# Kernel optimization log

Hardware: AMD Instinct MI355X
Metric: run time of the kernel (lower is better)

The kernel has to match this reference:

```python
import jax, jax.numpy as jnp
import numpy as np

D_MODEL = 1024
EXPAND = 2
D_INNER = D_MODEL * EXPAND  # 2048
D_STATE = 16
D_CONV = 4
B, T = 4, 2048


def setup_inputs() -> dict:
    key = jax.random.key(0)
    ks = jax.random.split(key, 8)
    s = 0.02  # small init std for numeric stability
    return {
        "x": jax.random.normal(ks[0], (B, T, D_MODEL), jnp.float32),
        "in_proj_w": jax.random.normal(ks[1], (2 * D_INNER, D_MODEL), jnp.float32) * s,
        "conv_w": jax.random.normal(ks[2], (D_INNER, 1, D_CONV), jnp.float32) * s,
        "conv_b": jnp.zeros((D_INNER,), jnp.float32),
        "x_proj_w": jax.random.normal(ks[3], (2 * D_STATE, D_INNER), jnp.float32) * s,
        "dt_proj_w": jax.random.normal(ks[4], (D_INNER, D_STATE), jnp.float32) * s,
        "dt_proj_b": jnp.zeros((D_INNER,), jnp.float32),
        "D_param": jnp.ones((D_INNER,), jnp.float32),
        "out_proj_w": jax.random.normal(ks[5], (D_MODEL, D_INNER), jnp.float32) * s,
    }


def reference(x, in_proj_w, conv_w, conv_b, x_proj_w, dt_proj_w, dt_proj_b, D_param, out_proj_w):
    Bsz, Tlen, _ = x.shape
    # in_proj (no bias), torch Linear: x @ W.T
    xz = jnp.einsum('btd,ed->bte', x, in_proj_w)            # [B,T,2*D_INNER]
    x_inner, z = jnp.split(xz, 2, axis=-1)                   # each [B,T,D_INNER]
    # depthwise causal conv1d: left-pad d_conv-1, take first T outputs
    xc = jnp.transpose(x_inner, (0, 2, 1))                   # [B,D_INNER,T]
    xc = jax.lax.conv_general_dilated(
        xc, conv_w, window_strides=(1,), padding=[(D_CONV - 1, 0)],
        feature_group_count=D_INNER)
    xc = xc + conv_b[None, :, None]
    x_conv = jax.nn.silu(jnp.transpose(xc, (0, 2, 1)))       # [B,T,D_INNER]
    # x_proj -> (B_ssm, C_ssm); C_ssm is unused by the simplified scan (faithful)
    x_ssm = jnp.einsum('btd,ed->bte', x_conv, x_proj_w)      # [B,T,2*D_STATE]
    B_ssm, C_ssm = jnp.split(x_ssm, 2, axis=-1)
    dt = jax.nn.softplus(jnp.einsum('btn,dn->btd', B_ssm, dt_proj_w) + dt_proj_b)  # [B,T,D_INNER]
    # simplified selective scan: EMA with scalar-per-timestep gate
    alpha = jax.nn.sigmoid(jnp.mean(dt, axis=-1, keepdims=True))  # [B,T,1]

    def step(h, inp):
        a, xt = inp
        h = a * h + (1.0 - a) * xt
        return h, h

    aT = jnp.transpose(alpha, (1, 0, 2))   # [T,B,1]
    xT = jnp.transpose(x_conv, (1, 0, 2))  # [T,B,D_INNER]
    h0 = jnp.zeros((Bsz, D_INNER), x.dtype)
    _, ys = jax.lax.scan(step, h0, (aT, xT))
    y = jnp.transpose(ys, (1, 0, 2))        # [B,T,D_INNER]
    y = y * D_param + x_conv                # skip with learned D
    y = y * jax.nn.silu(z)                  # gate
    out = jnp.einsum('btd,ed->bte', y, out_proj_w)  # [B,T,D_MODEL]
    return out
```

## Files before the change

kernel.cpp:

```cpp
#include <hip/hip_runtime.h>
#include <stdint.h>

#define TLEN   2048
#define DMODEL 1024
#define DINNER 2048
#define MROWS  8192
#define NCH    64
#define CHUNK  32

typedef unsigned short u16;
typedef __bf16 bf16x8 __attribute__((ext_vector_type(8)));
typedef float  f32x4  __attribute__((ext_vector_type(4)));

__device__ __forceinline__ float bf2f(u16 u) {
  union { unsigned int i; float f; } v; v.i = ((unsigned int)u) << 16; return v.f;
}
__device__ __forceinline__ u16 f2bf(float f) {
  union { float f; unsigned int u; } v; v.f = f;
  unsigned int u = v.u;
  return (u16)((u + 0x7fffu + ((u >> 16) & 1u)) >> 16);
}
__device__ __forceinline__ float silu_f(float x) { return x / (1.f + __expf(-x)); }

__device__ __forceinline__ void async16(const u16* g, u16* l) {
  __builtin_amdgcn_global_load_lds(
      (const __attribute__((address_space(1))) void*)(g),
      (__attribute__((address_space(3))) void*)(l),
      16, 0, 0);
}

#define BAR      asm volatile("s_barrier" ::: "memory")
#define WAITV(n) asm volatile("s_waitcnt vmcnt(" #n ")" ::: "memory")
#define PRIO1    __builtin_amdgcn_s_setprio(1)
#define PRIO0    __builtin_amdgcn_s_setprio(0)

__global__ __launch_bounds__(256) void k_convert(const float* __restrict__ x,
    const float* __restrict__ w1, const float* __restrict__ w3,
    const float* __restrict__ xpw,
    u16* __restrict__ xb, u16* __restrict__ w1b, u16* __restrict__ w3b,
    u16* __restrict__ xpwb) {
  int i = blockIdx.x * 256 + threadIdx.x;
  const int nx  = MROWS * DMODEL / 4;
  const int nw1 = 2 * DINNER * DMODEL / 4;
  const int nw3 = DMODEL * DINNER / 4;
  const float* src; u16* dst; int j;
  if (i < nx)                  { src = x;   dst = xb;   j = i; }
  else if (i < nx + nw1)       { src = w1;  dst = w1b;  j = i - nx; }
  else if (i < nx + nw1 + nw3) { src = w3;  dst = w3b;  j = i - nx - nw1; }
  else                         { src = xpw; dst = xpwb; j = i - nx - nw1 - nw3; }
  float4 v = ((const float4*)src)[j];
  ushort4 o;
  o.x = f2bf(v.x); o.y = f2bf(v.y); o.z = f2bf(v.z); o.w = f2bf(v.w);
  ((ushort4*)dst)[j] = o;
}

__device__ __forceinline__ u16* regp(u16* lds, int s, int mat, int h) {
  return lds + (((s * 2 + mat) * 2 + h) * 8192);
}

__device__ __forceinline__ void read_a(bf16x8 (&dst)[4][2], const u16* reg,
                                       int qa, int fr, int c0, int c1) {
  #pragma unroll
  for (int m = 0; m < 4; m++) {
    const u16* p = reg + (qa * 64 + m * 16 + fr) * 64;
    dst[m][0] = *(const bf16x8*)(p + c0);
    dst[m][1] = *(const bf16x8*)(p + c1);
  }
}
__device__ __forceinline__ void read_b(bf16x8 (&dst)[2][2], const u16* reg,
                                       int rb, int c0, int c1) {
  #pragma unroll
  for (int n = 0; n < 2; n++) {
    const u16* p = reg + (rb + n * 16) * 64;
    dst[n][0] = *(const bf16x8*)(p + c0);
    dst[n][1] = *(const bf16x8*)(p + c1);
  }
}
__device__ __forceinline__ void mfma_quad(f32x4 (&acc)[8][4],
    const bf16x8 (&af)[4][2], const bf16x8 (&bf)[2][2], int qa, int qb) {
  #pragma unroll
  for (int m = 0; m < 4; m++)
    #pragma unroll
    for (int n = 0; n < 2; n++)
      #pragma unroll
      for (int ks = 0; ks < 2; ks++)
        acc[qa * 4 + m][qb * 2 + n] = __builtin_amdgcn_mfma_f32_16x16x32_bf16(
            af[m][ks], bf[n][ks], acc[qa * 4 + m][qb * 2 + n], 0, 0, 0);
}

template<int N, int K, bool OUT_BF16>
__global__ __launch_bounds__(512) void k_gemm8p(const u16* __restrict__ A,
    const u16* __restrict__ Bm, void* __restrict__ C) {
  static_assert(K % 128 == 0, "K must be multiple of 128");
  extern __shared__ u16 lds[];
  const int tid  = threadIdx.x;
  const int lane = tid & 63;
  const int wave = tid >> 6;
  const int wm   = wave >> 2;
  const int wn   = wave & 3;
  const int fr   = lane & 15;
  const int q    = lane >> 4;

  int wg = blockIdx.x, nwg = gridDim.x, swz = wg;
  if ((nwg & 7) == 0) swz = (wg & 7) * (nwg >> 3) + (wg >> 3);
  const int NT_N = N / 256;
  const size_t blockM = (size_t)(swz / NT_N) * 256;
  const size_t blockN = (size_t)(swz % NT_N) * 256;

  const int rsub   = tid >> 3;
  const int srcCol = 8 * ((tid & 7) ^ (rsub & 7));
  const u16* gA = A  + (blockM + rsub) * (size_t)K + srcCol;
  const u16* gB = Bm + (blockN + rsub) * (size_t)K + srcCol;

#define STAGE(sl, mat, h, kt) do {                                           \
    const u16* _g = ((mat) ? gB : gA) + (size_t)(h) * (128 * (size_t)K)      \
                    + (size_t)(kt) * 64;                                     \
    u16* _l = regp(lds, (sl), (mat), (h)) + tid * 8;                         \
    async16(_g, _l);                                                         \
    async16(_g + (size_t)64 * K, _l + 4096);                                 \
  } while (0)

  const int c0 = (((q * 16)      ^ ((fr & 7) << 4)) >> 1);
  const int c1 = (((64 + q * 16) ^ ((fr & 7) << 4)) >> 1);
  const int rb = (wn & 1) * 64 + fr;

  f32x4 acc[8][4] = {};
  bf16x8 a0[4][2], a1[4][2], bl[2][2], bh[2][2];

  const int NT = K / 64;
  const int NITER = K / 128;

  STAGE(0, 0, 0, 0); STAGE(0, 0, 1, 0); STAGE(0, 1, 0, 0); STAGE(0, 1, 1, 0);
  STAGE(1, 1, 0, 1); STAGE(1, 1, 1, 1); STAGE(1, 0, 0, 1);
  WAITV(6);
  BAR;

  for (int it = 0; it < NITER; ++it) {
    const int t2 = 2 * it + 2, t3 = 2 * it + 3;
    const bool pf = (t2 < NT);
    read_a(a0, regp(lds, 0, 0, wm), 0, fr, c0, c1);
    read_b(bl, regp(lds, 0, 1, wn >> 1), rb, c0, c1);
    STAGE(1, 0, 1, 2 * it + 1);
    BAR;
    PRIO1; mfma_quad(acc, a0, bl, 0, 0); PRIO0;
    BAR;
    read_b(bh, regp(lds, 0, 1, wn >> 1), rb + 32, c0, c1);
    if (pf) STAGE(0, 1, 0, t2);
    BAR;
    PRIO1; mfma_quad(acc, a0, bh, 0, 1); PRIO0;
    BAR;
    read_a(a1, regp(lds, 0, 0, wm), 1, fr, c0, c1);
    if (pf) STAGE(0, 1, 1, t2);
    BAR;
    PRIO1; mfma_quad(acc, a1, bl, 1, 0); PRIO0;
    BAR;
    if (pf) STAGE(0, 0, 0, t2);
    BAR;
    PRIO1; mfma_quad(acc, a1, bh, 1, 1); PRIO0;
    if (pf) { WAITV(6); } else { WAITV(0); }
    BAR;
    read_a(a0, regp(lds, 1, 0, wm), 0, fr, c0, c1);
    read_b(bl, regp(lds, 1, 1, wn >> 1), rb, c0, c1);
    if (pf) STAGE(0, 0, 1, t2);
    BAR;
    PRIO1; mfma_quad(acc, a0, bl, 0, 0); PRIO0;
    BAR;
    read_b(bh, regp(lds, 1, 1, wn >> 1), rb + 32, c0, c1);
    if (pf) STAGE(1, 1, 0, t3);
    BAR;
    PRIO1; mfma_quad(acc, a0, bh, 0, 1); PRIO0;
    BAR;
    read_a(a1, regp(lds, 1, 0, wm), 1, fr, c0, c1);
    if (pf) STAGE(1, 1, 1, t3);
    BAR;
    PRIO1; mfma_quad(acc, a1, bl, 1, 0); PRIO0;
    BAR;
    if (pf) STAGE(1, 0, 0, t3);
    BAR;
    PRIO1; mfma_quad(acc, a1, bh, 1, 1); PRIO0;
    if (pf) { WAITV(6); BAR; } else { BAR; }
  }
#undef STAGE

  {
    const size_t r0  = blockM + (size_t)wm * 128;
    const size_t cc0 = blockN + (size_t)wn * 64;
    #pragma unroll
    for (int m = 0; m < 8; m++)
      #pragma unroll
      for (int n = 0; n < 4; n++)
        #pragma unroll
        for (int r = 0; r < 4; r++) {
          size_t row = r0 + m * 16 + q * 4 + r;
          size_t col = cc0 + n * 16 + fr;
          float v = acc[m][n][r];
          if (OUT_BF16) ((u16*)C)[row * N + col] = f2bf(v);
          else          ((float*)C)[row * N + col] = v;
        }
  }
}

template<int N, int K, bool OUT_BF16>
__global__ __launch_bounds__(512) void k_gemm_sk(const u16* __restrict__ A,
    const u16* __restrict__ B, void* __restrict__ C) {
  __shared__ u16 smem[2][2][2][4096];
  const int tid   = threadIdx.x;
  const int lane  = tid & 63;
  const int wave8 = tid >> 6;
  const int kw    = wave8 >> 2;
  const int wave  = wave8 & 3;
  const int wm    = (wave >> 1) * 64;
  const int wn    = (wave & 1) * 64;
  const int fr    = lane & 15;
  const int q     = lane >> 4;
  const size_t blockM = (size_t)blockIdx.y * 128;
  const size_t blockN = (size_t)blockIdx.x * 128;

  const int srow = lane >> 2;
  const int scol = (lane & 3) * 8;
  const size_t kbase = (size_t)kw * (K / 2);
  const u16* gA = A + (blockM + (size_t)wave * 32 + srow) * (size_t)K + kbase + scol;
  const u16* gB = B + (blockN + (size_t)wave * 32 + srow) * (size_t)K + kbase + scol;
  u16* lA0 = smem[kw][0][0] + wave * 1024;
  u16* lA1 = smem[kw][0][1] + wave * 1024;
  u16* lB0 = smem[kw][1][0] + wave * 1024;
  u16* lB1 = smem[kw][1][1] + wave * 1024;

  f32x4 acc[4][4] = {};

  for (int kt = 0; kt < K / 2; kt += 64) {
    async16(gA + kt,                        lA0);
    async16(gA + 16 * (size_t)K + kt,       lA0 + 512);
    async16(gA + kt + 32,                   lA1);
    async16(gA + 16 * (size_t)K + kt + 32,  lA1 + 512);
    async16(gB + kt,                        lB0);
    async16(gB + 16 * (size_t)K + kt,       lB0 + 512);
    async16(gB + kt + 32,                   lB1);
    async16(gB + 16 * (size_t)K + kt + 32,  lB1 + 512);
    __syncthreads();

    #pragma unroll
    for (int h = 0; h < 2; h++) {
      bf16x8 af[4], bfr[4];
      #pragma unroll
      for (int tm = 0; tm < 4; tm++)
        af[tm] = *(const bf16x8*)(smem[kw][0][h] + (wm + tm * 16 + fr) * 32 + q * 8);
      #pragma unroll
      for (int tn = 0; tn < 4; tn++)
        bfr[tn] = *(const bf16x8*)(smem[kw][1][h] + (wn + tn * 16 + fr) * 32 + q * 8);
      #pragma unroll
      for (int tm = 0; tm < 4; tm++)
        #pragma unroll
        for (int tn = 0; tn < 4; tn++)
          acc[tm][tn] = __builtin_amdgcn_mfma_f32_16x16x32_bf16(
              af[tm], bfr[tn], acc[tm][tn], 0, 0, 0);
    }
    __syncthreads();
  }

  float* red = (float*)smem;
  if (kw == 1) {
    const int t2 = tid - 256;
    #pragma unroll
    for (int tm = 0; tm < 4; tm++)
      #pragma unroll
      for (int tn = 0; tn < 4; tn++)
        #pragma unroll
        for (int r = 0; r < 4; r++)
          red[((t2 * 4 + tm) * 4 + tn) * 4 + r] = acc[tm][tn][r];
  }
  __syncthreads();
  if (kw == 0) {
    #pragma unroll
    for (int tm = 0; tm < 4; tm++)
      #pragma unroll
      for (int tn = 0; tn < 4; tn++)
        #pragma unroll
        for (int r = 0; r < 4; r++) {
          float v = acc[tm][tn][r] + red[((tid * 4 + tm) * 4 + tn) * 4 + r];
          size_t row = blockM + wm + tm * 16 + q * 4 + r;
          size_t col = blockN + wn + tn * 16 + fr;
          if (OUT_BF16) ((u16*)C)[row * N + col] = f2bf(v);
          else          ((float*)C)[row * N + col] = v;
        }
  }
}

__global__ __launch_bounds__(256) void k_conv(const u16* __restrict__ xz,
    const float* __restrict__ cw, const float* __restrict__ cb,
    u16* __restrict__ xc) {
  const int tb = blockIdx.x & 255;
  const int b  = blockIdx.x >> 8;
  const int d0 = threadIdx.x * 8;

  float wgt[8][4], bias[8];
  #pragma unroll
  for (int j = 0; j < 8; j++) {
    float4 wv = ((const float4*)cw)[d0 + j];
    wgt[j][0] = wv.x; wgt[j][1] = wv.y; wgt[j][2] = wv.z; wgt[j][3] = wv.w;
    bias[j] = cb[d0 + j];
  }

  const int t0 = tb * 8;
  const u16* base = xz + ((size_t)(b * TLEN + t0)) * 4096 + d0;
  float win[3][8];
  #pragma unroll
  for (int k = 0; k < 3; k++) {
    const int t = t0 - 3 + k;
    if (t >= 0) {
      bf16x8 v = *(const bf16x8*)(base + (ptrdiff_t)(k - 3) * 4096);
      #pragma unroll
      for (int j = 0; j < 8; j++) win[k][j] = bf2f(((u16*)&v)[j]);
    } else {
      #pragma unroll
      for (int j = 0; j < 8; j++) win[k][j] = 0.f;
    }
  }

  u16* outp = xc + ((size_t)(b * TLEN + t0)) * DINNER + d0;
  #pragma unroll
  for (int i = 0; i < 8; i++) {
    bf16x8 v = *(const bf16x8*)(base + (ptrdiff_t)i * 4096);
    float cur[8];
    #pragma unroll
    for (int j = 0; j < 8; j++) cur[j] = bf2f(((u16*)&v)[j]);
    union { u16 a[8]; int4 v4; } o;
    #pragma unroll
    for (int j = 0; j < 8; j++) {
      float acc = bias[j] + wgt[j][0] * win[0][j] + wgt[j][1] * win[1][j]
                + wgt[j][2] * win[2][j] + wgt[j][3] * cur[j];
      o.a[j] = f2bf(silu_f(acc));
    }
    *(int4*)(outp + (size_t)i * DINNER) = o.v4;
    #pragma unroll
    for (int j = 0; j < 8; j++) { win[0][j] = win[1][j]; win[1][j] = win[2][j]; win[2][j] = cur[j]; }
  }
}

__global__ __launch_bounds__(256) void k_bssm(const u16* __restrict__ xc,
    const u16* __restrict__ xpwb, float* __restrict__ bssm) {
  const int tid  = threadIdx.x;
  const int lane = tid & 63;
  const int wave = tid >> 6;
  const int fr   = lane & 15;
  const int q    = lane >> 4;
  const size_t row0 = (size_t)blockIdx.x * 32;
  const int k0 = wave * 512;

  f32x4 acc[2] = {};
  #pragma unroll
  for (int kk = 0; kk < 512; kk += 32) {
    const int kb = k0 + kk + q * 8;
    bf16x8 bfrag = *(const bf16x8*)(xpwb + (size_t)fr * DINNER + kb);
    #pragma unroll
    for (int tm = 0; tm < 2; tm++) {
      bf16x8 afrag = *(const bf16x8*)(xc + (row0 + tm * 16 + fr) * (size_t)DINNER + kb);
      acc[tm] = __builtin_amdgcn_mfma_f32_16x16x32_bf16(afrag, bfrag, acc[tm], 0, 0, 0);
    }
  }

  __shared__ float red[4][32][16];
  #pragma unroll
  for (int tm = 0; tm < 2; tm++)
    #pragma unroll
    for (int r = 0; r < 4; r++)
      red[wave][tm * 16 + q * 4 + r][fr] = acc[tm][r];
  __syncthreads();
  #pragma unroll
  for (int i = tid; i < 512; i += 256) {
    int r = i >> 4, n = i & 15;
    bssm[(row0 + r) * 16 + n] =
        red[0][r][n] + red[1][r][n] + red[2][r][n] + red[3][r][n];
  }
}

__global__ __launch_bounds__(256) void k_alpha(const float* __restrict__ bssm,
    const float* __restrict__ dtw, const float* __restrict__ dtb,
    float* __restrict__ alpha) {
  const int tid = threadIdx.x;
  const size_t row0 = (size_t)blockIdx.x * 16;
  __shared__ float4 sB[16][4];
  { int r = tid >> 4, n = tid & 15;
    ((float*)&sB[r][0])[n] = bssm[(row0 + r) * 16 + n]; }
  __syncthreads();

  float rowsum[16];
  #pragma unroll
  for (int r = 0; r < 16; r++) rowsum[r] = 0.f;

  #pragma unroll 1
  for (int m = 0; m < 4; m++) {
    const int d0 = m * 512 + tid * 2;
    float4 w[2][4]; float bias[2];
    #pragma unroll
    for (int j = 0; j < 2; j++) {
      const float4* wp = (const float4*)(dtw + (size_t)(d0 + j) * 16);
      w[j][0] = wp[0]; w[j][1] = wp[1]; w[j][2] = wp[2]; w[j][3] = wp[3];
      bias[j] = dtb[d0 + j];
    }
    #pragma unroll
    for (int r = 0; r < 16; r++) {
      float4 b0 = sB[r][0], b1 = sB[r][1], b2 = sB[r][2], b3 = sB[r][3];
      float s = 0.f;
      #pragma unroll
      for (int j = 0; j < 2; j++) {
        float dot = bias[j]
          + b0.x * w[j][0].x + b0.y * w[j][0].y + b0.z * w[j][0].z + b0.w * w[j][0].w
          + b1.x * w[j][1].x + b1.y * w[j][1].y + b1.z * w[j][1].z + b1.w * w[j][1].w
          + b2.x * w[j][2].x + b2.y * w[j][2].y + b2.z * w[j][2].z + b2.w * w[j][2].w
          + b3.x * w[j][3].x + b3.y * w[j][3].y + b3.z * w[j][3].z + b3.w * w[j][3].w;
        s += (dot > 15.f) ? dot : __logf(1.f + __expf(dot));
      }
      rowsum[r] += s;
    }
  }
  #pragma unroll
  for (int r = 0; r < 16; r++)
    #pragma unroll
    for (int off = 32; off > 0; off >>= 1) rowsum[r] += __shfl_xor(rowsum[r], off);
  __shared__ float red[4][16];
  if ((tid & 63) == 0) {
    #pragma unroll
    for (int r = 0; r < 16; r++) red[tid >> 6][r] = rowsum[r];
  }
  __syncthreads();
  if (tid < 16) {
    float mean = (red[0][tid] + red[1][tid] + red[2][tid] + red[3][tid]) * (1.f / DINNER);
    alpha[row0 + tid] = 1.f / (1.f + __expf(-mean));
  }
}

__global__ __launch_bounds__(256) void k_scan1(const u16* __restrict__ xc,
    const float* __restrict__ alpha, float* __restrict__ carry) {
  const int c = blockIdx.x & 63;
  const int b = blockIdx.x >> 6;
  const int d0 = threadIdx.x * 8;
  __shared__ float sa[CHUNK];
  if (threadIdx.x < CHUNK) sa[threadIdx.x] = alpha[b * TLEN + c * CHUNK + threadIdx.x];
  __syncthreads();
  const u16* xp = xc + ((size_t)(b * TLEN + c * CHUNK)) * DINNER + d0;
  float h[8];
  #pragma unroll
  for (int j = 0; j < 8; j++) h[j] = 0.f;
  #pragma unroll 4
  for (int i = 0; i < CHUNK; i++) {
    bf16x8 v = *(const bf16x8*)(xp + (size_t)i * DINNER);
    float a = sa[i];
    #pragma unroll
    for (int j = 0; j < 8; j++) h[j] = a * h[j] + (1.f - a) * bf2f(((u16*)&v)[j]);
  }
  float* cp = carry + ((size_t)(b * NCH + c)) * DINNER + d0;
  #pragma unroll
  for (int j = 0; j < 8; j++) cp[j] = h[j];
}

__global__ __launch_bounds__(256) void k_scan2(float* __restrict__ carry,
    const float* __restrict__ alpha) {
  int i = blockIdx.x * 256 + threadIdx.x;
  int b = i >> 11;
  int d = i & (DINNER - 1);
  __shared__ float sP[NCH];
  if (threadIdx.x < NCH) {
    const float* ap = alpha + b * TLEN + threadIdx.x * CHUNK;
    float p = 1.f;
    for (int j = 0; j < CHUNK; j++) p *= ap[j];
    sP[threadIdx.x] = p;
  }
  __syncthreads();
  float h = 0.f;
  #pragma unroll
  for (int c = 0; c < NCH; c++) {
    size_t idx = ((size_t)(b * NCH + c)) * DINNER + d;
    float cv = carry[idx];
    carry[idx] = h;
    h = sP[c] * h + cv;
  }
}

__global__ __launch_bounds__(256) void k_scan3(const u16* __restrict__ xc,
    const u16* __restrict__ xz, const float* __restrict__ alpha,
    const float* __restrict__ Hs, const float* __restrict__ Dp,
    u16* __restrict__ yg) {
  const int c = blockIdx.x & 63;
  const int b = blockIdx.x >> 6;
  const int d0 = threadIdx.x * 8;
  __shared__ float sa[CHUNK];
  if (threadIdx.x < CHUNK) sa[threadIdx.x] = alpha[b * TLEN + c * CHUNK + threadIdx.x];
  __syncthreads();
  float h[8], Dv[8];
  { const float* hp = Hs + ((size_t)(b * NCH + c)) * DINNER + d0;
    #pragma unroll
    for (int j = 0; j < 8; j++) { h[j] = hp[j]; Dv[j] = Dp[d0 + j]; } }
  const size_t row0 = (size_t)(b * TLEN + c * CHUNK);
  #pragma unroll 2
  for (int i = 0; i < CHUNK; i++) {
    const size_t row = row0 + i;
    bf16x8 xv8 = *(const bf16x8*)(xc + row * DINNER + d0);
    bf16x8 zv8 = *(const bf16x8*)(xz + row * 4096 + DINNER + d0);
    const float a = sa[i];
    union { u16 o[8]; int4 v4; } out;
    #pragma unroll
    for (int j = 0; j < 8; j++) {
      float xv = bf2f(((u16*)&xv8)[j]);
      float zv = bf2f(((u16*)&zv8)[j]);
      h[j] = a * h[j] + (1.f - a) * xv;
      float y = h[j] * Dv[j] + xv;
      out.o[j] = f2bf(y * silu_f(zv));
    }
    *(int4*)(yg + row * DINNER + d0) = out.v4;
  }
}

extern "C" void kernel_launch(void* const* d_in, const int* in_sizes, int n_in,
                              void* d_out, int out_size, void* d_ws, size_t ws_size,
                              hipStream_t stream) {
  const float* x   = (const float*)d_in[0];
  const float* w1  = (const float*)d_in[1];
  const float* cw  = (const float*)d_in[2];
  const float* cb  = (const float*)d_in[3];
  const float* xpw = (const float*)d_in[4];
  const float* dtw = (const float*)d_in[5];
  const float* dtb = (const float*)d_in[6];
  const float* Dp  = (const float*)d_in[7];
  const float* w3  = (const float*)d_in[8];
  float* out = (float*)d_out;
  char* ws = (char*)d_ws;

  u16*   xb    = (u16*)(ws + 0);
  u16*   w1b   = (u16*)(ws + 16777216);
  u16*   w3b   = (u16*)(ws + 25165824);
  u16*   xz    = (u16*)(ws + 29360128);
  u16*   xc    = (u16*)(ws + 96468992);
  u16*   yg    = (u16*)(ws + 130023424);
  float* bssm  = (float*)(ws + 163577856);
  float* alpha = (float*)(ws + 164102144);
  float* carry = (float*)(ws + 0);
  u16*   xpwb  = (u16*)(ws + 164659456);

  k_convert<<<14368, 256, 0, stream>>>(x, w1, w3, xpw, xb, w1b, w3b, xpwb);
  k_gemm8p<4096, 1024, true><<<512, 512, 131072, stream>>>(xb, w1b, xz);
  k_conv   <<<1024, 256, 0, stream>>>(xz, cw, cb, xc);
  k_bssm   <<<256, 256, 0, stream>>>(xc, xpwb, bssm);
  k_alpha  <<<512, 256, 0, stream>>>(bssm, dtw, dtb, alpha);
  k_scan1  <<<256, 256, 0, stream>>>(xc, alpha, carry);
  k_scan2  <<<32, 256, 0, stream>>>(carry, alpha);
  k_scan3  <<<256, 256, 0, stream>>>(xc, xz, alpha, carry, Dp, yg);
  k_gemm_sk<1024, 2048, false><<<dim3(8, 64), 512, 0, stream>>>(yg, w3b, out);
}
```

Baseline: 327.7 us.

## Replace split-K out_proj GEMM with 128x64 tile kernel; batch scan2 carry loads

The out_proj GEMM drops its intra-block split-K with LDS reduction. It now uses a 256-thread kernel with 128x64 output tiles over the full K, which doubles the grid to 1024 blocks and removes the reduction pass and its extra synchronisation. The trade-off is a longer K loop per block and less B-tile reuse. Separately, k_scan2 preloads all 64 carry values into registers before the sequential recurrence, so the loads are issued back-to-back instead of interleaved with dependent updates.

Measured after the change: 339.1 us. 3.5% more time.

```diff
diff --git a/kernel.cpp b/kernel.cpp
--- a/kernel.cpp
+++ b/kernel.cpp
@@ -200,90 +200,70 @@
   }
 }
 
-template<int N, int K, bool OUT_BF16>
-__global__ __launch_bounds__(512) void k_gemm_sk(const u16* __restrict__ A,
-    const u16* __restrict__ B, void* __restrict__ C) {
-  __shared__ u16 smem[2][2][2][4096];
-  const int tid   = threadIdx.x;
-  const int lane  = tid & 63;
-  const int wave8 = tid >> 6;
-  const int kw    = wave8 >> 2;
-  const int wave  = wave8 & 3;
-  const int wm    = (wave >> 1) * 64;
-  const int wn    = (wave & 1) * 64;
-  const int fr    = lane & 15;
-  const int q     = lane >> 4;
+template<int N, int K>
+__global__ __launch_bounds__(256) void k_gemm2(const u16* __restrict__ A,
+    const u16* __restrict__ B, float* __restrict__ C) {
+  __shared__ u16 sA[2][128 * 32];
+  __shared__ u16 sB[2][64 * 32];
+  const int tid  = threadIdx.x;
+  const int lane = tid & 63;
+  const int wave = tid >> 6;
+  const int wm   = (wave >> 1) * 64;
+  const int wn   = (wave & 1) * 32;
+  const int fr   = lane & 15;
+  const int q    = lane >> 4;
   const size_t blockM = (size_t)blockIdx.y * 128;
-  const size_t blockN = (size_t)blockIdx.x * 128;
+  const size_t blockN = (size_t)blockIdx.x * 64;
 
   const int srow = lane >> 2;
   const int scol = (lane & 3) * 8;
-  const size_t kbase = (size_t)kw * (K / 2);
-  const u16* gA = A + (blockM + (size_t)wave * 32 + srow) * (size_t)K + kbase + scol;
-  const u16* gB = B + (blockN + (size_t)wave * 32 + srow) * (size_t)K + kbase + scol;
-  u16* lA0 = smem[kw][0][0] + wave * 1024;
-  u16* lA1 = smem[kw][0][1] + wave * 1024;
-  u16* lB0 = smem[kw][1][0] + wave * 1024;
-  u16* lB1 = smem[kw][1][1] + wave * 1024;
-
-  f32x4 acc[4][4] = {};
-
-  for (int kt = 0; kt < K / 2; kt += 64) {
+  const u16* gA = A + (blockM + (size_t)wave * 32 + srow) * (size_t)K + scol;
+  const u16* gB = B + (blockN + (size_t)wave * 16 + srow) * (size_t)K + scol;
+  u16* lA0 = sA[0] + wave * 1024;
+  u16* lA1 = sA[1] + wave * 1024;
+  u16* lB0 = sB[0] + wave * 512;
+  u16* lB1 = sB[1] + wave * 512;
+
+  f32x4 acc[4][2] = {};
+
+  for (int kt = 0; kt < K; kt += 64) {
     async16(gA + kt,                        lA0);
     async16(gA + 16 * (size_t)K + kt,       lA0 + 512);
     async16(gA + kt + 32,                   lA1);
     async16(gA + 16 * (size_t)K + kt + 32,  lA1 + 512);
     async16(gB + kt,                        lB0);
-    async16(gB + 16 * (size_t)K + kt,       lB0 + 512);
     async16(gB + kt + 32,                   lB1);
-    async16(gB + 16 * (size_t)K + kt + 32,  lB1 + 512);
     __syncthreads();
 
     #pragma unroll
     for (int h = 0; h < 2; h++) {
-      bf16x8 af[4], bfr[4];
+      bf16x8 af[4], bfr[2];
       #pragma unroll
       for (int tm = 0; tm < 4; tm++)
-        af[tm] = *(const bf16x8*)(smem[kw][0][h] + (wm + tm * 16 + fr) * 32 + q * 8);
-      #pragma unroll
-      for (int tn = 0; tn < 4; tn++)
-        bfr[tn] = *(const bf16x8*)(smem[kw][1][h] + (wn + tn * 16 + fr) * 32 + q * 8);
+        af[tm] = *(const bf16x8*)(sA[h] + (wm + tm * 16 + fr) * 32 + q * 8);
+      #pragma unroll
+      for (int tn = 0; tn < 2; tn++)
+        bfr[tn] = *(const bf16x8*)(sB[h] + (wn + tn * 16 + fr) * 32 + q * 8);
       #pragma unroll
       for (int tm = 0; tm < 4; tm++)
         #pragma unroll
-        for (int tn = 0; tn < 4; tn++)
+        for (int tn = 0; tn < 2; tn++)
           acc[tm][tn] = __builtin_amdgcn_mfma_f32_16x16x32_bf16(
               af[tm], bfr[tn], acc[tm][tn], 0, 0, 0);
     }
     __syncthreads();
   }
 
-  float* red = (float*)smem;
-  if (kw == 1) {
-    const int t2 = tid - 256;
-    #pragma unroll
-    for (int tm = 0; tm < 4; tm++)
-      #pragma unroll
-      for (int tn = 0; tn < 4; tn++)
-        #pragma unroll
-        for (int r = 0; r < 4; r++)
-          red[((t2 * 4 + tm) * 4 + tn) * 4 + r] = acc[tm][tn][r];
-  }
-  __syncthreads();
-  if (kw == 0) {
-    #pragma unroll
-    for (int tm = 0; tm < 4; tm++)
-      #pragma unroll
-      for (int tn = 0; tn < 4; tn++)
-        #pragma unroll
-        for (int r = 0; r < 4; r++) {
-          float v = acc[tm][tn][r] + red[((tid * 4 + tm) * 4 + tn) * 4 + r];
-          size_t row = blockM + wm + tm * 16 + q * 4 + r;
-          size_t col = blockN + wn + tn * 16 + fr;
-          if (OUT_BF16) ((u16*)C)[row * N + col] = f2bf(v);
-          else          ((float*)C)[row * N + col] = v;
-        }
-  }
+  #pragma unroll
+  for (int tm = 0; tm < 4; tm++)
+    #pragma unroll
+    for (int tn = 0; tn < 2; tn++)
+      #pragma unroll
+      for (int r = 0; r < 4; r++) {
+        size_t row = blockM + wm + tm * 16 + q * 4 + r;
+        size_t col = blockN + wn + tn * 16 + fr;
+        C[row * N + col] = acc[tm][tn][r];
+      }
 }
 
 __global__ __launch_bounds__(256) void k_conv(const u16* __restrict__ xz,
@@ -467,13 +447,15 @@
     sP[threadIdx.x] = p;
   }
   __syncthreads();
+  float* base = carry + (size_t)b * NCH * DINNER + d;
+  float cv[NCH];
+  #pragma unroll
+  for (int c = 0; c < NCH; c++) cv[c] = base[(size_t)c * DINNER];
   float h = 0.f;
   #pragma unroll
   for (int c = 0; c < NCH; c++) {
-    size_t idx = ((size_t)(b * NCH + c)) * DINNER + d;
-    float cv = carry[idx];
-    carry[idx] = h;
-    h = sP[c] * h + cv;
+    base[(size_t)c * DINNER] = h;
+    h = sP[c] * h + cv[c];
   }
 }
 
@@ -545,5 +527,5 @@
   k_scan1  <<<256, 256, 0, stream>>>(xc, alpha, carry);
   k_scan2  <<<32, 256, 0, stream>>>(carry, alpha);
   k_scan3  <<<256, 256, 0, stream>>>(xc, xz, alpha, carry, Dp, yg);
-  k_gemm_sk<1024, 2048, false><<<dim3(8, 64), 512, 0, stream>>>(yg, w3b, out);
-}
+  k_gemm2<1024, 2048><<<dim3(16, 64), 256, 0, stream>>>(yg, w3b, out);
+}
```
